# Performance work log

Hardware: AMD Instinct MI355X
Metric: run time of the kernel (lower is better)

## Reference

```python
import jax, jax.numpy as jnp
import numpy as np

N, E, H, RBF, NZ = 15000, 300000, 128, 20, 119
CUTOFF, BOX = 6.0, 7.0


def setup_inputs() -> dict:
    key = jax.random.key(0)
    ks = jax.random.split(key, 24)
    s = 0.05

    def rn(k, shape):
        return jax.random.normal(k, shape, dtype=jnp.float32) * s

    z = jax.random.randint(ks[0], (N,), 0, 83)
    pos = jax.random.uniform(ks[1], (N, 3), dtype=jnp.float32) * BOX
    src = jax.random.randint(ks[2], (E,), 0, N)
    dst = (src + jax.random.randint(ks[3], (E,), 1, N)) % N  # guarantees src != dst
    edge_index = jnp.stack([src, dst], axis=0)  # (2, E)
    cell_offsets = (jax.random.randint(ks[4], (E, 3), 0, 3) - 1).astype(jnp.float32)
    cell = jnp.eye(3, dtype=jnp.float32) * BOX
    return dict(
        z=z, pos=pos, edge_index=edge_index, cell_offsets=cell_offsets, cell=cell,
        embed=rn(ks[5], (NZ, H)),
        msg_w1=rn(ks[6], (3, H, H)), msg_b1=rn(ks[7], (3, H)),
        msg_w2=rn(ks[8], (3, H, 3 * H)), msg_b2=rn(ks[9], (3, 3 * H)),
        filt_w=rn(ks[10], (3, RBF, 3 * H)), filt_b=rn(ks[11], (3, 3 * H)),
        upd_uw=rn(ks[12], (3, H, H)), upd_ub=rn(ks[13], (3, H)),
        upd_vw=rn(ks[14], (3, H, H)), upd_vb=rn(ks[15], (3, H)),
        upd_mw1=rn(ks[16], (3, 2 * H, H)), upd_mb1=rn(ks[17], (3, H)),
        upd_mw2=rn(ks[18], (3, H, 3 * H)), upd_mb2=rn(ks[19], (3, 3 * H)),
        head_w1=rn(ks[20], (H, H)), head_b1=rn(ks[21], (H,)),
        head_w2=rn(ks[22], (H, H)), head_b2=rn(ks[23], (H,)),
    )


def reference(z, pos, edge_index, cell_offsets, cell, embed,
              msg_w1, msg_b1, msg_w2, msg_b2, filt_w, filt_b,
              upd_uw, upd_ub, upd_vw, upd_vb,
              upd_mw1, upd_mb1, upd_mw2, upd_mb2,
              head_w1, head_b1, head_w2, head_b2):
    n_nodes = z.shape[0]
    hdim = embed.shape[1]
    row, col = edge_index[0], edge_index[1]  # receiver, sender (DeepDFT convention)

    # get_pbc_distances
    offsets = cell_offsets @ cell                                  # (E,3)
    edge_diff = pos[row] - pos[col] + offsets                      # (E,3)
    edge_dist = jnp.linalg.norm(edge_diff, axis=-1)                # (E,)
    unit = edge_diff / edge_dist[:, None]                          # (E,3)

    # sinc radial basis + cosine cutoff (shared by all message layers)
    n = jnp.arange(1, RBF + 1, dtype=pos.dtype)
    rbf = jnp.sin(edge_dist[:, None] * n * jnp.pi / CUTOFF) / edge_dist[:, None]  # (E,RBF)
    fcut = jnp.where(edge_dist < CUTOFF,
                     0.5 * (jnp.cos(jnp.pi * edge_dist / CUTOFF) + 1.0), 0.0)      # (E,)

    ns = embed[z]                                                  # (N,H)
    nv = jnp.zeros((n_nodes, 3, hdim), dtype=pos.dtype)            # (N,3,H)

    for i in range(3):
        # ---- PainnMessage ----
        filt = (rbf @ filt_w[i] + filt_b[i]) * fcut[:, None]       # (E,3H)
        sout = jax.nn.silu(ns @ msg_w1[i] + msg_b1[i]) @ msg_w2[i] + msg_b2[i]  # (N,3H)
        fo = filt * sout[col]                                      # (E,3H)
        gate_v, gate_e, msg_s = jnp.split(fo, 3, axis=1)           # each (E,H)
        msg_v = nv[col] * gate_v[:, None, :] + gate_e[:, None, :] * unit[:, :, None]  # (E,3,H)
        ns = ns + jax.ops.segment_sum(msg_s, row, num_segments=n_nodes)
        nv = nv + jax.ops.segment_sum(msg_v, row, num_segments=n_nodes)
        # ---- PainnUpdate ----
        Uv = nv @ upd_uw[i] + upd_ub[i]                            # (N,3,H)
        Vv = nv @ upd_vw[i] + upd_vb[i]                            # (N,3,H)
        mlp_in = jnp.concatenate([jnp.linalg.norm(Vv, axis=1), ns], axis=1)  # (N,2H)
        m = jax.nn.silu(mlp_in @ upd_mw1[i] + upd_mb1[i]) @ upd_mw2[i] + upd_mb2[i]  # (N,3H)
        a_vv, a_sv, a_ss = jnp.split(m, 3, axis=1)
        inner = jnp.sum(Uv * Vv, axis=1)                           # (N,H)
        nv = nv + a_vv[:, None, :] * Uv
        ns = ns + a_sv * inner + a_ss

    v = jax.nn.silu(ns @ head_w1 + head_b1) @ head_w2 + head_b2    # (N,H)
    return v, edge_dist
```

## Files before the change

kernel.cpp:

```cpp
#include <hip/hip_runtime.h>
#include <math.h>

#define HD 128
#define H3 384
#define RBF_N 20
#define CUTOFF_R 6.0f
#define PI_F 3.14159265358979323846f
#define CAPE 40000

#define PITCH 136

typedef __attribute__((ext_vector_type(8))) short short8v;
typedef __attribute__((ext_vector_type(4))) short short4v;
typedef __attribute__((ext_vector_type(4))) float f32x4;
typedef unsigned short bf_t;

__device__ __forceinline__ float silu_f(float x) { return x / (1.0f + __expf(-x)); }

__device__ __forceinline__ ushort f2bf(float f) {
    union { float f; uint u; } v; v.f = f;
    return (ushort)((v.u + 0x7FFF + ((v.u >> 16) & 1)) >> 16);
}
__device__ __forceinline__ float bf2f(ushort x) {
    union { uint u; float f; } v; v.u = ((uint)x) << 16;
    return v.f;
}
__device__ __forceinline__ short4v f2bf4(float4 x) {
    short4v r;
    r[0] = (short)f2bf(x.x); r[1] = (short)f2bf(x.y);
    r[2] = (short)f2bf(x.z); r[3] = (short)f2bf(x.w);
    return r;
}
__device__ __forceinline__ float4 b2f4(short4v x) {
    return make_float4(bf2f((ushort)x[0]), bf2f((ushort)x[1]),
                       bf2f((ushort)x[2]), bf2f((ushort)x[3]));
}

#define LOADWG(r, CNT, NTH, W, rowlen, koff)                                   \
    _Pragma("unroll")                                                          \
    for (int it_ = 0; it_ < CNT; ++it_) {                                      \
        int u_ = tid + it_ * NTH;                                              \
        (r)[it_] = *(const short8v*)((W) + (size_t)(u_ >> 4) * (rowlen) +      \
                                     (koff) + ((u_ & 15) << 3));               \
    }
#define COMMITWG(r, CNT, NTH)                                                  \
    _Pragma("unroll")                                                          \
    for (int it_ = 0; it_ < CNT; ++it_) {                                      \
        int u_ = tid + it_ * NTH;                                              \
        *(short8v*)&Wt[(u_ >> 4) * PITCH + ((u_ & 15) << 3)] = (r)[it_];       \
    }
#define MFMA4R(Abuf, acc)                                                      \
    _Pragma("unroll")                                                          \
    for (int step_ = 0; step_ < 4; ++step_) {                                  \
        int kb_ = step_ * 32 + lk;                                             \
        short8v a_ = *(const short8v*)&(Abuf)[(wr + lr) * PITCH + kb_];        \
        (acc) = __builtin_amdgcn_mfma_f32_16x16x32_bf16(                       \
            a_, *(const short8v*)&Wt[(wn + lr) * PITCH + kb_], (acc), 0, 0, 0);\
    }
#define MFMA8R(Abuf, acc)                                                      \
    _Pragma("unroll")                                                          \
    for (int step_ = 0; step_ < 4; ++step_) {                                  \
        int kb_ = step_ * 32 + lk;                                             \
        short8v a_ = *(const short8v*)&(Abuf)[(wr + lr) * PITCH + kb_];        \
        (acc)[0] = __builtin_amdgcn_mfma_f32_16x16x32_bf16(                    \
            a_, *(const short8v*)&Wt[(wn + lr) * PITCH + kb_], (acc)[0], 0, 0, 0); \
        (acc)[1] = __builtin_amdgcn_mfma_f32_16x16x32_bf16(                    \
            a_, *(const short8v*)&Wt[(wn + 16 + lr) * PITCH + kb_], (acc)[1], 0, 0, 0); \
    }

__global__ void geom_kernel(const float* __restrict__ pos, const int* __restrict__ ei,
                            const float* __restrict__ cofs, const float* __restrict__ cell,
                            float* __restrict__ dist_out, int* __restrict__ deg, int E) {
    int e = blockIdx.x * blockDim.x + threadIdx.x;
    if (e >= E) return;
    int r = ei[e], c = ei[E + e];
    float c0 = cofs[3*e], c1 = cofs[3*e+1], c2 = cofs[3*e+2];
    float d0 = pos[3*r]   - pos[3*c]   + c0*cell[0] + c1*cell[3] + c2*cell[6];
    float d1 = pos[3*r+1] - pos[3*c+1] + c0*cell[1] + c1*cell[4] + c2*cell[7];
    float d2 = pos[3*r+2] - pos[3*c+2] + c0*cell[2] + c1*cell[5] + c2*cell[8];
    float dist = sqrtf(d0*d0 + d1*d1 + d2*d2);
    dist_out[e] = dist;
    if (dist < CUTOFF_R) atomicAdd(&deg[r], 1);
}

__global__ void scan_kernel(const int* __restrict__ deg, int* __restrict__ off,
                            int* __restrict__ cursor, int n) {
    __shared__ int wsum[16];
    __shared__ int carry_s;
    const int tid = threadIdx.x;
    const int lane = tid & 63, wv = tid >> 6;
    if (tid == 0) carry_s = 0;
    __syncthreads();
    for (int base = 0; base < n; base += 1024) {
        int v = (base + tid < n) ? deg[base + tid] : 0;
        int x = v;
        #pragma unroll
        for (int s = 1; s < 64; s <<= 1) {
            int y = __shfl_up(x, s);
            if (lane >= s) x += y;
        }
        if (lane == 63) wsum[wv] = x;
        __syncthreads();
        if (tid == 0) {
            int a = carry_s;
            #pragma unroll
            for (int i = 0; i < 16; ++i) { int t = wsum[i]; wsum[i] = a; a += t; }
            carry_s = a;
        }
        __syncthreads();
        int exc = wsum[wv] + x - v;
        if (base + tid < n) { off[base + tid] = exc; cursor[base + tid] = exc; }
        __syncthreads();
    }
    if (tid == 0) off[n] = carry_s;
}

__global__ void scatter_kernel(const float* __restrict__ pos, const int* __restrict__ ei,
                               const float* __restrict__ cofs, const float* __restrict__ cell,
                               const float* __restrict__ dist_in, int* __restrict__ cursor,
                               int* __restrict__ col_s, float* __restrict__ fcut_s,
                               float* __restrict__ unit_s, float* __restrict__ rbf_s, int E) {
    int e = blockIdx.x * blockDim.x + threadIdx.x;
    if (e >= E) return;
    float dist = dist_in[e];
    if (!(dist < CUTOFF_R)) return;
    int r = ei[e], c = ei[E + e];
    float c0 = cofs[3*e], c1 = cofs[3*e+1], c2 = cofs[3*e+2];
    float d0 = pos[3*r]   - pos[3*c]   + c0*cell[0] + c1*cell[3] + c2*cell[6];
    float d1 = pos[3*r+1] - pos[3*c+1] + c0*cell[1] + c1*cell[4] + c2*cell[7];
    float d2 = pos[3*r+2] - pos[3*c+2] + c0*cell[2] + c1*cell[5] + c2*cell[8];
    int p = atomicAdd(&cursor[r], 1);
    if (p >= CAPE) return;
    col_s[p] = c;
    fcut_s[p] = 0.5f * (cosf(PI_F * dist / CUTOFF_R) + 1.0f);
    float inv = 1.0f / dist;
    unit_s[3*p]   = d0 * inv;
    unit_s[3*p+1] = d1 * inv;
    unit_s[3*p+2] = d2 * inv;
    #pragma unroll
    for (int j = 0; j < RBF_N; ++j)
        rbf_s[(size_t)p*RBF_N + j] = sinf(dist * (float)(j+1) * (PI_F / CUTOFF_R)) * inv;
}

__device__ __forceinline__ void wcvt(const float* __restrict__ src, bf_t* __restrict__ dst,
                                     int idx, int K, int N) {
    int per = K * N;
    int l = idx / per, r = idx % per;
    int k = r / N, n = r % N;
    dst[(size_t)l*per + (size_t)n*K + k] = f2bf(src[(size_t)l*per + (size_t)k*N + n]);
}

__global__ void wprep_kernel(const float* s0, const float* s1, const float* s2, const float* s3,
                             const float* s4, const float* s5, const float* s6, const float* s7,
                             bf_t* __restrict__ dst) {
    int i = blockIdx.x * blockDim.x + threadIdx.x;
    if (i < 49152)        wcvt(s0, dst + 0,      i - 0,      128, 128);
    else if (i < 196608)  wcvt(s1, dst + 49152,  i - 49152,  128, 384);
    else if (i < 245760)  wcvt(s2, dst + 196608, i - 196608, 128, 128);
    else if (i < 294912)  wcvt(s3, dst + 245760, i - 245760, 128, 128);
    else if (i < 393216)  wcvt(s4, dst + 294912, i - 294912, 256, 128);
    else if (i < 540672)  wcvt(s5, dst + 393216, i - 393216, 128, 384);
    else if (i < 557056)  wcvt(s6, dst + 540672, i - 540672, 128, 128);
    else if (i < 573440)  wcvt(s7, dst + 557056, i - 557056, 128, 128);
}

__global__ __launch_bounds__(512) void msg_mlp0(const int* __restrict__ z,
                                                const float* __restrict__ emb,
                                                bf_t* __restrict__ nsb,
                                                const bf_t* __restrict__ W1b,
                                                const float* __restrict__ b1,
                                                const bf_t* __restrict__ W2b,
                                                const float* __restrict__ b2,
                                                bf_t* __restrict__ Cb, int M) {
    __shared__ ushort As[32 * PITCH];
    __shared__ ushort Wt[128 * PITCH];
    __shared__ ushort Hid[32 * PITCH];
    const int tid = threadIdx.x;
    const int m0 = blockIdx.x * 32;
    const int wid = tid >> 6, lane = tid & 63;
    const int wr = (wid >> 2) * 16;
    const int wn = (wid & 3) * 32;
    const int lr = lane & 15, lk = (lane >> 4) << 3;
    const int er = (lane >> 4) << 2;

    short8v rwA[4], rwB[4];
    LOADWG(rwA, 4, 512, W1b, 128, 0);
    {
        int row = tid >> 4, k8 = (tid & 15) << 3;
        int m = m0 + row;
        short8v pk = (short8v)(0);
        if (m < M) {
            const float* ep = emb + (size_t)z[m] * HD + k8;
            const float4 x = *(const float4*)ep, y = *(const float4*)(ep + 4);
            pk[0]=(short)f2bf(x.x); pk[1]=(short)f2bf(x.y);
            pk[2]=(short)f2bf(x.z); pk[3]=(short)f2bf(x.w);
            pk[4]=(short)f2bf(y.x); pk[5]=(short)f2bf(y.y);
            pk[6]=(short)f2bf(y.z); pk[7]=(short)f2bf(y.w);
            *(short8v*)(nsb + (size_t)m * HD + k8) = pk;
        }
        *(short8v*)&As[row * PITCH + k8] = pk;
    }
    __syncthreads();
    COMMITWG(rwA, 4, 512); LOADWG(rwB, 4, 512, W2b, 128, 0);
    __syncthreads();
    f32x4 acc1[2];
    acc1[0] = (f32x4)(0.f); acc1[1] = (f32x4)(0.f);
    MFMA8R(As, acc1);
    __syncthreads();
    COMMITWG(rwB, 4, 512); LOADWG(rwA, 4, 512, W2b + 16384, 128, 0);
    #pragma unroll
    for (int j = 0; j < 2; ++j) {
        int col = wn + 16 * j + lr;
        float bb = b1[col];
        #pragma unroll
        for (int r = 0; r < 4; ++r)
            Hid[(wr + er + r) * PITCH + col] = f2bf(silu_f(acc1[j][r] + bb));
    }
    __syncthreads();
    {
        f32x4 a0[2]; a0[0] = (f32x4)(0.f); a0[1] = (f32x4)(0.f);
        MFMA8R(Hid, a0);
        __syncthreads();
        COMMITWG(rwA, 4, 512); LOADWG(rwB, 4, 512, W2b + 32768, 128, 0);
        #pragma unroll
        for (int j = 0; j < 2; ++j) {
            int col = wn + 16 * j + lr;
            float bb = b2[col];
            #pragma unroll
            for (int r = 0; r < 4; ++r) {
                int m = m0 + wr + er + r;
                if (m < M) Cb[(size_t)m * H3 + col] = f2bf(a0[j][r] + bb);
            }
        }
        __syncthreads();
    }
    {
        f32x4 a1[2]; a1[0] = (f32x4)(0.f); a1[1] = (f32x4)(0.f);
        MFMA8R(Hid, a1);
        __syncthreads();
        COMMITWG(rwB, 4, 512);
        #pragma unroll
        for (int j = 0; j < 2; ++j) {
            int col = wn + 16 * j + lr;
            float bb = b2[128 + col];
            #pragma unroll
            for (int r = 0; r < 4; ++r) {
                int m = m0 + wr + er + r;
                if (m < M) Cb[(size_t)m * H3 + 128 + col] = f2bf(a1[j][r] + bb);
            }
        }
        __syncthreads();
    }
    {
        f32x4 a2[2]; a2[0] = (f32x4)(0.f); a2[1] = (f32x4)(0.f);
        MFMA8R(Hid, a2);
        #pragma unroll
        for (int j = 0; j < 2; ++j) {
            int col = wn + 16 * j + lr;
            float bb = b2[256 + col];
            #pragma unroll
            for (int r = 0; r < 4; ++r) {
                int m = m0 + wr + er + r;
                if (m < M) Cb[(size_t)m * H3 + 256 + col] = f2bf(a2[j][r] + bb);
            }
        }
    }
}

template <int MODE>
__global__ __launch_bounds__(1024) void upd_fused(const bf_t* __restrict__ nv2p,
                                                 const bf_t* __restrict__ Ub,
                                                 const bf_t* __restrict__ Vb,
                                                 const float* __restrict__ bu,
                                                 const float* __restrict__ bv,
                                                 bf_t* __restrict__ nvp,
                                                 bf_t* __restrict__ nsb,
                                                 const bf_t* __restrict__ W1b,
                                                 const float* __restrict__ b1,
                                                 const bf_t* __restrict__ W2b,
                                                 const float* __restrict__ b2,
                                                 const bf_t* __restrict__ xw1,
                                                 const float* __restrict__ xb1,
                                                 const bf_t* __restrict__ xw2,
                                                 const float* __restrict__ xb2,
                                                 bf_t* __restrict__ soutb,
                                                 float* __restrict__ Cf,
                                                 int N) {
    __shared__ ushort As3[3][32 * PITCH];
    __shared__ ushort Wt[128 * PITCH];
    __shared__ ushort nrmL[32 * PITCH];
    __shared__ ushort Hid[32 * PITCH];
    __shared__ ushort AsG[32 * PITCH];
    const int tid = threadIdx.x;
    const int m0 = blockIdx.x * 32;
    const int wid = tid >> 6, lane = tid & 63;
    const int wr = (wid >> 3) * 16;
    const int wn = (wid & 7) * 16;
    const int lr = lane & 15, lk = (lane >> 4) << 3;
    const int er = (lane >> 4) << 2;
    const size_t NHD = (size_t)N * HD;

    short8v rwA[2], rwB[2];
    LOADWG(rwA, 2, 1024, Ub, 128, 0);

    #pragma unroll
    for (int it = 0; it < 2; ++it) {
        int u = tid + it * 1024;
        if (u < 1536) {
            int d = u >> 9, v = u & 511;
            int row = v >> 4, k8 = (v & 15) << 3;
            int m = m0 + row;
            short8v pk = (short8v)(0);
            if (m < N) pk = *(const short8v*)(nv2p + (size_t)d * NHD + (size_t)m * HD + k8);
            *(short8v*)&As3[d][row * PITCH + k8] = pk;
        }
    }
    if (tid < 512) {
        int row = tid >> 4, k8 = (tid & 15) << 3;
        int m = m0 + row;
        short8v pk = (short8v)(0);
        if (m < N) pk = *(const short8v*)(nsb + (size_t)m * HD + k8);
        *(short8v*)&AsG[row * PITCH + k8] = pk;
    }
    __syncthreads();
    COMMITWG(rwA, 2, 1024); LOADWG(rwB, 2, 1024, Vb, 128, 0);
    __syncthreads();

    f32x4 aU[3], aV[3];
    #pragma unroll
    for (int d = 0; d < 3; ++d) { aU[d] = (f32x4)(0.f); aV[d] = (f32x4)(0.f); }
    #pragma unroll
    for (int d = 0; d < 3; ++d) { MFMA4R(As3[d], aU[d]); }
    __syncthreads();
    COMMITWG(rwB, 2, 1024); LOADWG(rwA, 2, 1024, W1b, 256, 0);
    __syncthreads();

    #pragma unroll
    for (int d = 0; d < 3; ++d) { MFMA4R(As3[d], aV[d]); }
    float inn_r[4];
    {
        int col = wn + lr;
        float bbu = bu[col], bbv = bv[col];
        #pragma unroll
        for (int r = 0; r < 4; ++r) {
            float inn = 0.f, nrm = 0.f;
            #pragma unroll
            for (int d = 0; d < 3; ++d) {
                float u = aU[d][r] + bbu;
                float v = aV[d][r] + bbv;
                aU[d][r] = u;
                inn += u * v;
                nrm += v * v;
            }
            inn_r[r] = inn;
            nrmL[(wr + er + r) * PITCH + col] = f2bf(sqrtf(nrm));
        }
    }
    __syncthreads();
    COMMITWG(rwA, 2, 1024); LOADWG(rwB, 2, 1024, W1b, 256, 128);
    __syncthreads();

    f32x4 acc1 = (f32x4)(0.f);
    MFMA4R(nrmL, acc1);
    __syncthreads();
    COMMITWG(rwB, 2, 1024);
    if (MODE == 1) { LOADWG(rwA, 2, 1024, W2b, 128, 0); }
    else           { LOADWG(rwA, 2, 1024, W2b + 16384, 128, 0); }
    __syncthreads();

    MFMA4R(AsG, acc1);
    {
        int col = wn + lr;
        float bb = b1[col];
        #pragma unroll
        for (int r = 0; r < 4; ++r)
            Hid[(wr + er + r) * PITCH + col] = f2bf(silu_f(acc1[r] + bb));
    }
    __syncthreads();
    COMMITWG(rwA, 2, 1024);
    if (MODE == 1) { LOADWG(rwB, 2, 1024, W2b + 16384, 128, 0); }
    else           { LOADWG(rwB, 2, 1024, W2b + 32768, 128, 0); }
    __syncthreads();

    float sv[4];
    if (MODE == 1) {
        f32x4 g0 = (f32x4)(0.f);
        MFMA4R(Hid, g0);
        {
            int col = wn + lr;
            float bb = b2[col];
            #pragma unroll
            for (int r = 0; r < 4; ++r) {
                int m = m0 + wr + er + r;
                if (m < N) {
                    float g = g0[r] + bb;
                    #pragma unroll
                    for (int d = 0; d < 3; ++d) {
                        float pp = bf2f(As3[d][(wr + er + r) * PITCH + col]);
                        nvp[(size_t)d * NHD + (size_t)m * HD + col] =
                            f2bf(pp + g * aU[d][r]);
                    }
                }
            }
        }
        __syncthreads();
        COMMITWG(rwB, 2, 1024); LOADWG(rwA, 2, 1024, W2b + 32768, 128, 0);
        __syncthreads();
        f32x4 g1 = (f32x4)(0.f);
        MFMA4R(Hid, g1);
        {
            int col = wn + lr;
            float bb = b2[128 + col];
            #pragma unroll
            for (int r = 0; r < 4; ++r)
                sv[r] = (g1[r] + bb) * inn_r[r];
        }
        __syncthreads();
        COMMITWG(rwA, 2, 1024); LOADWG(rwB, 2, 1024, xw1, 128, 0);
        __syncthreads();
        f32x4 g2 = (f32x4)(0.f);
        MFMA4R(Hid, g2);
        {
            int col = wn + lr;
            float bb = b2[256 + col];
            #pragma unroll
            for (int r = 0; r < 4; ++r) {
                int m = m0 + wr + er + r;
                if (m < N) {
                    int idx = (wr + er + r) * PITCH + col;
                    float s = bf2f(AsG[idx]) + sv[r] + (g2[r] + bb);
                    ushort sb = f2bf(s);
                    AsG[idx] = sb;
                    nsb[(size_t)m * HD + col] = sb;
                }
            }
        }
        __syncthreads();
        COMMITWG(rwB, 2, 1024); LOADWG(rwA, 2, 1024, xw2, 128, 0);
        __syncthreads();
        f32x4 ah = (f32x4)(0.f);
        MFMA4R(AsG, ah);
        {
            int col = wn + lr;
            float bb = xb1[col];
            #pragma unroll
            for (int r = 0; r < 4; ++r)
                Hid[(wr + er + r) * PITCH + col] = f2bf(silu_f(ah[r] + bb));
        }
        __syncthreads();
        COMMITWG(rwA, 2, 1024); LOADWG(rwB, 2, 1024, xw2 + 16384, 128, 0);
        __syncthreads();
        {
            f32x4 o0 = (f32x4)(0.f);
            MFMA4R(Hid, o0);
            int col = wn + lr;
            float bb = xb2[col];
            #pragma unroll
            for (int r = 0; r < 4; ++r) {
                int m = m0 + wr + er + r;
                if (m < N) soutb[(size_t)m * H3 + col] = f2bf(o0[r] + bb);
            }
        }
        __syncthreads();
        COMMITWG(rwB, 2, 1024); LOADWG(rwA, 2, 1024, xw2 + 32768, 128, 0);
        __syncthreads();
        {
            f32x4 o1 = (f32x4)(0.f);
            MFMA4R(Hid, o1);
            int col = wn + lr;
            float bb = xb2[128 + col];
            #pragma unroll
            for (int r = 0; r < 4; ++r) {
                int m = m0 + wr + er + r;
                if (m < N) soutb[(size_t)m * H3 + 128 + col] = f2bf(o1[r] + bb);
            }
        }
        __syncthreads();
        COMMITWG(rwA, 2, 1024);
        __syncthreads();
        {
            f32x4 o2 = (f32x4)(0.f);
            MFMA4R(Hid, o2);
            int col = wn + lr;
            float bb = xb2[256 + col];
            #pragma unroll
            for (int r = 0; r < 4; ++r) {
                int m = m0 + wr + er + r;
                if (m < N) soutb[(size_t)m * H3 + 256 + col] = f2bf(o2[r] + bb);
            }
        }
    } else {
        f32x4 g1 = (f32x4)(0.f);
        MFMA4R(Hid, g1);
        {
            int col = wn + lr;
            float bb = b2[128 + col];
            #pragma unroll
            for (int r = 0; r < 4; ++r)
                sv[r] = (g1[r] + bb) * inn_r[r];
        }
        __syncthreads();
        COMMITWG(rwB, 2, 1024); LOADWG(rwA, 2, 1024, xw1, 128, 0);
        __syncthreads();
        f32x4 g2 = (f32x4)(0.f);
        MFMA4R(Hid, g2);
        {
            int col = wn + lr;
            float bb = b2[256 + col];
            #pragma unroll
            for (int r = 0; r < 4; ++r) {
                int idx = (wr + er + r) * PITCH + col;
                float s = bf2f(AsG[idx]) + sv[r] + (g2[r] + bb);
                AsG[idx] = f2bf(s);
            }
        }
        __syncthreads();
        COMMITWG(rwA, 2, 1024); LOADWG(rwB, 2, 1024, xw2, 128, 0);
        __syncthreads();
        f32x4 ah = (f32x4)(0.f);
        MFMA4R(AsG, ah);
        {
            int col = wn + lr;
            float bb = xb1[col];
            #pragma unroll
            for (int r = 0; r < 4; ++r)
                Hid[(wr + er + r) * PITCH + col] = f2bf(silu_f(ah[r] + bb));
        }
        __syncthreads();
        COMMITWG(rwB, 2, 1024);
        __syncthreads();
        f32x4 ao = (f32x4)(0.f);
        MFMA4R(Hid, ao);
        {
            int col = wn + lr;
            float bb = xb2[col];
            #pragma unroll
            for (int r = 0; r < 4; ++r) {
                int m = m0 + wr + er + r;
                if (m < N) Cf[(size_t)m * HD + col] = ao[r] + bb;
            }
        }
    }
}

template <int FIRST>
__global__ __launch_bounds__(128) void message_kernel(
        bf_t* __restrict__ ns_b,
        const bf_t* __restrict__ nv_b, bf_t* __restrict__ nv2_b,
        const bf_t* __restrict__ sout,
        const int* __restrict__ col_s, const float* __restrict__ unit_s,
        const float* __restrict__ rbf_s, const float* __restrict__ fcut_s,
        const float* __restrict__ Wf_g, const float* __restrict__ bf_g,
        const int* __restrict__ off, int n_nodes) {
    const int t = threadIdx.x;
    const int nA = blockIdx.x * 2;
    if (nA >= n_nodes) return;
    const int nB = nA + 1;
    const bool hasB = (nB < n_nodes);
    const size_t NHD = (size_t)n_nodes * HD;

    float w0[RBF_N], w1[RBF_N], w2[RBF_N];
    #pragma unroll
    for (int r = 0; r < RBF_N; ++r) {
        w0[r] = Wf_g[r * H3 + t];
        w1[r] = Wf_g[r * H3 + HD + t];
        w2[r] = Wf_g[r * H3 + 2*HD + t];
    }
    const float bb0 = bf_g[t], bb1 = bf_g[HD + t], bb2 = bf_g[2*HD + t];

    int e0   = off[nA];
    int endA = off[nA + 1];
    int end  = hasB ? off[nB + 1] : endA;
    if (endA > CAPE) endA = CAPE;
    if (end  > CAPE) end  = CAPE;

    float aS = 0.f, a0 = 0.f, a1 = 0.f, a2 = 0.f;
    float bS = 0.f, b0 = 0.f, b1 = 0.f, b2 = 0.f;

    int e = e0;
    for (; e + 1 < end; e += 2) {
        int cX = col_s[e], cY = col_s[e + 1];
        float fcX = fcut_s[e], fcY = fcut_s[e + 1];
        float uX0 = unit_s[3*e],   uX1 = unit_s[3*e+1], uX2 = unit_s[3*e+2];
        float uY0 = unit_s[3*e+3], uY1 = unit_s[3*e+4], uY2 = unit_s[3*e+5];
        float fX0 = bb0, fX1 = bb1, fX2 = bb2;
        float fY0 = bb0, fY1 = bb1, fY2 = bb2;
        const float* rbX = rbf_s + (size_t)e * RBF_N;
        const float* rbY = rbX + RBF_N;
        #pragma unroll
        for (int r = 0; r < RBF_N; ++r) {
            float rx = rbX[r], ry = rbY[r];
            fX0 += rx * w0[r]; fY0 += ry * w0[r];
            fX1 += rx * w1[r]; fY1 += ry * w1[r];
            fX2 += rx * w2[r]; fY2 += ry * w2[r];
        }
        const bf_t* spX = sout + (size_t)cX * H3;
        const bf_t* spY = sout + (size_t)cY * H3;
        float gvX = fX0 * fcX * bf2f(spX[t]);
        float geX = fX1 * fcX * bf2f(spX[HD+t]);
        float msX = fX2 * fcX * bf2f(spX[2*HD+t]);
        float gvY = fY0 * fcY * bf2f(spY[t]);
        float geY = fY1 * fcY * bf2f(spY[HD+t]);
        float msY = fY2 * fcY * bf2f(spY[2*HD+t]);
        float vX0, vX1, vX2, vY0, vY1, vY2;
        if (FIRST) {
            vX0 = geX * uX0; vX1 = geX * uX1; vX2 = geX * uX2;
            vY0 = geY * uY0; vY1 = geY * uY1; vY2 = geY * uY2;
        } else {
            const bf_t* nvX = nv_b + (size_t)cX * HD + t;
            const bf_t* nvY = nv_b + (size_t)cY * HD + t;
            vX0 = bf2f(nvX[0])     * gvX + geX * uX0;
            vX1 = bf2f(nvX[NHD])   * gvX + geX * uX1;
            vX2 = bf2f(nvX[2*NHD]) * gvX + geX * uX2;
            vY0 = bf2f(nvY[0])     * gvY + geY * uY0;
            vY1 = bf2f(nvY[NHD])   * gvY + geY * uY1;
            vY2 = bf2f(nvY[2*NHD]) * gvY + geY * uY2;
        }
        if (e < endA) { a0 += vX0; a1 += vX1; a2 += vX2; aS += msX; }
        else          { b0 += vX0; b1 += vX1; b2 += vX2; bS += msX; }
        if (e + 1 < endA) { a0 += vY0; a1 += vY1; a2 += vY2; aS += msY; }
        else              { b0 += vY0; b1 += vY1; b2 += vY2; bS += msY; }
    }
    if (e < end) {
        int c = col_s[e];
        float fc = fcut_s[e];
        float u0 = unit_s[3*e], u1 = unit_s[3*e+1], u2 = unit_s[3*e+2];
        float f0 = bb0, f1 = bb1, f2 = bb2;
        const float* rb = rbf_s + (size_t)e * RBF_N;
        #pragma unroll
        for (int r = 0; r < RBF_N; ++r) {
            float rv = rb[r];
            f0 += rv * w0[r];
            f1 += rv * w1[r];
            f2 += rv * w2[r];
        }
        const bf_t* sp = sout + (size_t)c * H3;
        float gv = f0 * fc * bf2f(sp[t]);
        float ge = f1 * fc * bf2f(sp[HD+t]);
        float ms = f2 * fc * bf2f(sp[2*HD+t]);
        float v0, v1, v2;
        if (FIRST) {
            v0 = ge * u0; v1 = ge * u1; v2 = ge * u2;
        } else {
            const bf_t* nvc = nv_b + (size_t)c * HD + t;
            v0 = bf2f(nvc[0])     * gv + ge * u0;
            v1 = bf2f(nvc[NHD])   * gv + ge * u1;
            v2 = bf2f(nvc[2*NHD]) * gv + ge * u2;
        }
        if (e < endA) { a0 += v0; a1 += v1; a2 += v2; aS += ms; }
        else          { b0 += v0; b1 += v1; b2 += v2; bS += ms; }
    }

    {
        size_t b = (size_t)nA * HD + t;
        if (FIRST) {
            nv2_b[b]         = f2bf(a0);
            nv2_b[b + NHD]   = f2bf(a1);
            nv2_b[b + 2*NHD] = f2bf(a2);
        } else {
            nv2_b[b]         = f2bf(bf2f(nv_b[b])         + a0);
            nv2_b[b + NHD]   = f2bf(bf2f(nv_b[b + NHD])   + a1);
            nv2_b[b + 2*NHD] = f2bf(bf2f(nv_b[b + 2*NHD]) + a2);
        }
        if (endA > e0) {
            size_t so = (size_t)nA * HD + t;
            ns_b[so] = f2bf(bf2f(ns_b[so]) + aS);
        }
    }
    if (hasB) {
        size_t b = (size_t)nB * HD + t;
        if (FIRST) {
            nv2_b[b]         = f2bf(b0);
            nv2_b[b + NHD]   = f2bf(b1);
            nv2_b[b + 2*NHD] = f2bf(b2);
        } else {
            nv2_b[b]         = f2bf(bf2f(nv_b[b])         + b0);
            nv2_b[b + NHD]   = f2bf(bf2f(nv_b[b + NHD])   + b1);
            nv2_b[b + 2*NHD] = f2bf(bf2f(nv_b[b + 2*NHD]) + b2);
        }
        if (end > endA) {
            size_t so = (size_t)nB * HD + t;
            ns_b[so] = f2bf(bf2f(ns_b[so]) + bS);
        }
    }
}

extern "C" void kernel_launch(void* const* d_in, const int* in_sizes, int n_in,
                              void* d_out, int out_size, void* d_ws, size_t ws_size,
                              hipStream_t stream) {
    const int*   z       = (const int*)  d_in[0];
    const float* pos     = (const float*)d_in[1];
    const int*   ei      = (const int*)  d_in[2];
    const float* cofs    = (const float*)d_in[3];
    const float* cell    = (const float*)d_in[4];
    const float* emb     = (const float*)d_in[5];
    const float* msg_w1  = (const float*)d_in[6];
    const float* msg_b1  = (const float*)d_in[7];
    const float* msg_w2  = (const float*)d_in[8];
    const float* msg_b2  = (const float*)d_in[9];
    const float* filt_w  = (const float*)d_in[10];
    const float* filt_b  = (const float*)d_in[11];
    const float* upd_uw  = (const float*)d_in[12];
    const float* upd_ub  = (const float*)d_in[13];
    const float* upd_vw  = (const float*)d_in[14];
    const float* upd_vb  = (const float*)d_in[15];
    const float* upd_mw1 = (const float*)d_in[16];
    const float* upd_mb1 = (const float*)d_in[17];
    const float* upd_mw2 = (const float*)d_in[18];
    const float* upd_mb2 = (const float*)d_in[19];
    const float* head_w1 = (const float*)d_in[20];
    const float* head_b1 = (const float*)d_in[21];
    const float* head_w2 = (const float*)d_in[22];
    const float* head_b2 = (const float*)d_in[23];

    const int N = in_sizes[0];
    const int E = in_sizes[2] / 2;

    float* out_v    = (float*)d_out;
    float* out_dist = out_v + (size_t)N * HD;

    char* p = (char*)d_ws;
    auto alloc = [&](size_t bytes) -> void* {
        void* r = (void*)p;
        p += (bytes + 255) & ~(size_t)255;
        return r;
    };
    bf_t*  ns_b   = (bf_t*) alloc((size_t)N * HD * 2);
    bf_t*  nv_b   = (bf_t*) alloc((size_t)N * H3 * 2);
    bf_t*  nv2_b  = (bf_t*) alloc((size_t)N * H3 * 2);
    bf_t*  sout   = (bf_t*) alloc((size_t)N * H3 * 2);
    bf_t*  wb     = (bf_t*) alloc((size_t)573440 * 2);
    float* rbf_s  = (float*)alloc((size_t)CAPE * RBF_N * 4);
    float* fcut_s = (float*)alloc((size_t)CAPE * 4);
    float* unit_s = (float*)alloc((size_t)CAPE * 3 * 4);
    int*   col_s  = (int*)  alloc((size_t)CAPE * 4);
    int*   deg    = (int*)  alloc((size_t)N * 4);
    int*   off    = (int*)  alloc((size_t)(N + 1) * 4);
    int*   cursor = (int*)  alloc((size_t)N * 4);

    hipMemsetAsync(deg, 0, (size_t)N * 4, stream);

    int eb = (E + 255) / 256;
    geom_kernel<<<eb, 256, 0, stream>>>(pos, ei, cofs, cell, out_dist, deg, E);
    scan_kernel<<<1, 1024, 0, stream>>>(deg, off, cursor, N);
    scatter_kernel<<<eb, 256, 0, stream>>>(pos, ei, cofs, cell, out_dist, cursor,
                                           col_s, fcut_s, unit_s, rbf_s, E);
    wprep_kernel<<<(573440 + 255) / 256, 256, 0, stream>>>(
        msg_w1, msg_w2, upd_uw, upd_vw, upd_mw1, upd_mw2, head_w1, head_w2, wb);

    const bf_t* w_msg1 = wb + 0;
    const bf_t* w_msg2 = wb + 49152;
    const bf_t* w_uw   = wb + 196608;
    const bf_t* w_vw   = wb + 245760;
    const bf_t* w_mw1  = wb + 294912;
    const bf_t* w_mw2  = wb + 393216;
    const bf_t* w_hw1  = wb + 540672;
    const bf_t* w_hw2  = wb + 557056;

    int mt32 = (N + 31) / 32;
    int mpairs = (N + 1) / 2;

    msg_mlp0<<<mt32, 512, 0, stream>>>(
        z, emb, ns_b, w_msg1, msg_b1, w_msg2, msg_b2, sout, N);

    for (int i = 0; i < 3; ++i) {
        if (i == 0)
            message_kernel<1><<<mpairs, 128, 0, stream>>>(
                ns_b, nv_b, nv2_b, sout, col_s, unit_s, rbf_s, fcut_s,
                filt_w + (size_t)i*RBF_N*H3, filt_b + (size_t)i*H3, off, N);
        else
            message_kernel<0><<<mpairs, 128, 0, stream>>>(
                ns_b, nv_b, nv2_b, sout, col_s, unit_s, rbf_s, fcut_s,
                filt_w + (size_t)i*RBF_N*H3, filt_b + (size_t)i*H3, off, N);
        if (i < 2) {
            upd_fused<1><<<mt32, 1024, 0, stream>>>(
                nv2_b, w_uw + (size_t)i*16384, w_vw + (size_t)i*16384,
                upd_ub + (size_t)i*HD, upd_vb + (size_t)i*HD,
                nv_b, ns_b,
                w_mw1 + (size_t)i*32768, upd_mb1 + (size_t)i*HD,
                w_mw2 + (size_t)i*49152, upd_mb2 + (size_t)i*H3,
                w_msg1 + (size_t)(i+1)*16384, msg_b1 + (size_t)(i+1)*HD,
                w_msg2 + (size_t)(i+1)*49152, msg_b2 + (size_t)(i+1)*H3,
                sout, nullptr, N);
        } else {
            upd_fused<3><<<mt32, 1024, 0, stream>>>(
                nv2_b, w_uw + (size_t)i*16384, w_vw + (size_t)i*16384,
                upd_ub + (size_t)i*HD, upd_vb + (size_t)i*HD,
                nv_b, ns_b,
                w_mw1 + (size_t)i*32768, upd_mb1 + (size_t)i*HD,
                w_mw2 + (size_t)i*49152, upd_mb2 + (size_t)i*H3,
                w_hw1, head_b1, w_hw2, head_b2,
                nullptr, out_v, N);
        }
    }
}
```

Before: 225.5 us.

## Cache edge vectors, drop separate norm LDS buffer, store filter weights as bf16

```diff
diff --git a/kernel.cpp b/kernel.cpp
--- a/kernel.cpp
+++ b/kernel.cpp
@@ -70,7 +70,8 @@
 
 __global__ void geom_kernel(const float* __restrict__ pos, const int* __restrict__ ei,
                             const float* __restrict__ cofs, const float* __restrict__ cell,
-                            float* __restrict__ dist_out, int* __restrict__ deg, int E) {
+                            float* __restrict__ dist_out, float* __restrict__ dvec,
+                            int* __restrict__ deg, int E) {
     int e = blockIdx.x * blockDim.x + threadIdx.x;
     if (e >= E) return;
     int r = ei[e], c = ei[E + e];
@@ -80,7 +81,12 @@
     float d2 = pos[3*r+2] - pos[3*c+2] + c0*cell[2] + c1*cell[5] + c2*cell[8];
     float dist = sqrtf(d0*d0 + d1*d1 + d2*d2);
     dist_out[e] = dist;
-    if (dist < CUTOFF_R) atomicAdd(&deg[r], 1);
+    if (dist < CUTOFF_R) {
+        dvec[e]       = d0;
+        dvec[E + e]   = d1;
+        dvec[2*E + e] = d2;
+        atomicAdd(&deg[r], 1);
+    }
 }
 
 __global__ void scan_kernel(const int* __restrict__ deg, int* __restrict__ off,
@@ -115,9 +121,10 @@
     if (tid == 0) off[n] = carry_s;
 }
 
-__global__ void scatter_kernel(const float* __restrict__ pos, const int* __restrict__ ei,
-                               const float* __restrict__ cofs, const float* __restrict__ cell,
-                               const float* __restrict__ dist_in, int* __restrict__ cursor,
+__global__ void scatter_kernel(const int* __restrict__ ei,
+                               const float* __restrict__ dist_in,
+                               const float* __restrict__ dvec,
+                               int* __restrict__ cursor,
                                int* __restrict__ col_s, float* __restrict__ fcut_s,
                                float* __restrict__ unit_s, float* __restrict__ rbf_s, int E) {
     int e = blockIdx.x * blockDim.x + threadIdx.x;
@@ -125,10 +132,7 @@
     float dist = dist_in[e];
     if (!(dist < CUTOFF_R)) return;
     int r = ei[e], c = ei[E + e];
-    float c0 = cofs[3*e], c1 = cofs[3*e+1], c2 = cofs[3*e+2];
-    float d0 = pos[3*r]   - pos[3*c]   + c0*cell[0] + c1*cell[3] + c2*cell[6];
-    float d1 = pos[3*r+1] - pos[3*c+1] + c0*cell[1] + c1*cell[4] + c2*cell[7];
-    float d2 = pos[3*r+2] - pos[3*c+2] + c0*cell[2] + c1*cell[5] + c2*cell[8];
+    float d0 = dvec[e], d1 = dvec[E + e], d2 = dvec[2*E + e];
     int p = atomicAdd(&cursor[r], 1);
     if (p >= CAPE) return;
     col_s[p] = c;
@@ -152,6 +156,7 @@
 
 __global__ void wprep_kernel(const float* s0, const float* s1, const float* s2, const float* s3,
                              const float* s4, const float* s5, const float* s6, const float* s7,
+                             const float* s8,
                              bf_t* __restrict__ dst) {
     int i = blockIdx.x * blockDim.x + threadIdx.x;
     if (i < 49152)        wcvt(s0, dst + 0,      i - 0,      128, 128);
@@ -162,6 +167,7 @@
     else if (i < 540672)  wcvt(s5, dst + 393216, i - 393216, 128, 384);
     else if (i < 557056)  wcvt(s6, dst + 540672, i - 540672, 128, 128);
     else if (i < 573440)  wcvt(s7, dst + 557056, i - 557056, 128, 128);
+    else if (i < 596480)  dst[i] = f2bf(s8[i - 573440]);
 }
 
 __global__ __launch_bounds__(512) void msg_mlp0(const int* __restrict__ z,
@@ -288,7 +294,6 @@
                                                  int N) {
     __shared__ ushort As3[3][32 * PITCH];
     __shared__ ushort Wt[128 * PITCH];
-    __shared__ ushort nrmL[32 * PITCH];
     __shared__ ushort Hid[32 * PITCH];
     __shared__ ushort AsG[32 * PITCH];
     const int tid = threadIdx.x;
@@ -353,7 +358,7 @@
                 nrm += v * v;
             }
             inn_r[r] = inn;
-            nrmL[(wr + er + r) * PITCH + col] = f2bf(sqrtf(nrm));
+            Hid[(wr + er + r) * PITCH + col] = f2bf(sqrtf(nrm));
         }
     }
     __syncthreads();
@@ -361,7 +366,7 @@
     __syncthreads();
 
     f32x4 acc1 = (f32x4)(0.f);
-    MFMA4R(nrmL, acc1);
+    MFMA4R(Hid, acc1);
     __syncthreads();
     COMMITWG(rwB, 2, 1024);
     if (MODE == 1) { LOADWG(rwA, 2, 1024, W2b, 128, 0); }
@@ -440,6 +445,7 @@
         __syncthreads();
         f32x4 ah = (f32x4)(0.f);
         MFMA4R(AsG, ah);
+        __syncthreads();
         {
             int col = wn + lr;
             float bb = xb1[col];
@@ -519,6 +525,7 @@
         __syncthreads();
         f32x4 ah = (f32x4)(0.f);
         MFMA4R(AsG, ah);
+        __syncthreads();
         {
             int col = wn + lr;
             float bb = xb1[col];
@@ -550,7 +557,7 @@
         const bf_t* __restrict__ sout,
         const int* __restrict__ col_s, const float* __restrict__ unit_s,
         const float* __restrict__ rbf_s, const float* __restrict__ fcut_s,
-        const float* __restrict__ Wf_g, const float* __restrict__ bf_g,
+        const bf_t* __restrict__ Wf_b, const float* __restrict__ bf_g,
         const int* __restrict__ off, int n_nodes) {
     const int t = threadIdx.x;
     const int nA = blockIdx.x * 2;
@@ -562,9 +569,9 @@
     float w0[RBF_N], w1[RBF_N], w2[RBF_N];
     #pragma unroll
     for (int r = 0; r < RBF_N; ++r) {
-        w0[r] = Wf_g[r * H3 + t];
-        w1[r] = Wf_g[r * H3 + HD + t];
-        w2[r] = Wf_g[r * H3 + 2*HD + t];
+        w0[r] = bf2f(Wf_b[r * H3 + t]);
+        w1[r] = bf2f(Wf_b[r * H3 + HD + t]);
+        w2[r] = bf2f(Wf_b[r * H3 + 2*HD + t]);
     }
     const float bb0 = bf_g[t], bb1 = bf_g[HD + t], bb2 = bf_g[2*HD + t];
 
@@ -729,7 +736,8 @@
     bf_t*  nv_b   = (bf_t*) alloc((size_t)N * H3 * 2);
     bf_t*  nv2_b  = (bf_t*) alloc((size_t)N * H3 * 2);
     bf_t*  sout   = (bf_t*) alloc((size_t)N * H3 * 2);
-    bf_t*  wb     = (bf_t*) alloc((size_t)573440 * 2);
+    bf_t*  wb     = (bf_t*) alloc((size_t)596480 * 2);
+    float* dvec   = (float*)alloc((size_t)E * 3 * 4);
     float* rbf_s  = (float*)alloc((size_t)CAPE * RBF_N * 4);
     float* fcut_s = (float*)alloc((size_t)CAPE * 4);
     float* unit_s = (float*)alloc((size_t)CAPE * 3 * 4);
@@ -741,12 +749,12 @@
     hipMemsetAsync(deg, 0, (size_t)N * 4, stream);
 
     int eb = (E + 255) / 256;
-    geom_kernel<<<eb, 256, 0, stream>>>(pos, ei, cofs, cell, out_dist, deg, E);
+    geom_kernel<<<eb, 256, 0, stream>>>(pos, ei, cofs, cell, out_dist, dvec, deg, E);
     scan_kernel<<<1, 1024, 0, stream>>>(deg, off, cursor, N);
-    scatter_kernel<<<eb, 256, 0, stream>>>(pos, ei, cofs, cell, out_dist, cursor,
+    scatter_kernel<<<eb, 256, 0, stream>>>(ei, out_dist, dvec, cursor,
                                            col_s, fcut_s, unit_s, rbf_s, E);
-    wprep_kernel<<<(573440 + 255) / 256, 256, 0, stream>>>(
-        msg_w1, msg_w2, upd_uw, upd_vw, upd_mw1, upd_mw2, head_w1, head_w2, wb);
+    wprep_kernel<<<(596480 + 255) / 256, 256, 0, stream>>>(
+        msg_w1, msg_w2, upd_uw, upd_vw, upd_mw1, upd_mw2, head_w1, head_w2, filt_w, wb);
 
     const bf_t* w_msg1 = wb + 0;
     const bf_t* w_msg2 = wb + 49152;
@@ -756,6 +764,7 @@
     const bf_t* w_mw2  = wb + 393216;
     const bf_t* w_hw1  = wb + 540672;
     const bf_t* w_hw2  = wb + 557056;
+    const bf_t* w_fw   = wb + 573440;
 
     int mt32 = (N + 31) / 32;
     int mpairs = (N + 1) / 2;
@@ -767,11 +776,11 @@
         if (i == 0)
             message_kernel<1><<<mpairs, 128, 0, stream>>>(
                 ns_b, nv_b, nv2_b, sout, col_s, unit_s, rbf_s, fcut_s,
-                filt_w + (size_t)i*RBF_N*H3, filt_b + (size_t)i*H3, off, N);
+                w_fw + (size_t)i*RBF_N*H3, filt_b + (size_t)i*H3, off, N);
         else
             message_kernel<0><<<mpairs, 128, 0, stream>>>(
                 ns_b, nv_b, nv2_b, sout, col_s, unit_s, rbf_s, fcut_s,
-                filt_w + (size_t)i*RBF_N*H3, filt_b + (size_t)i*H3, off, N);
+                w_fw + (size_t)i*RBF_N*H3, filt_b + (size_t)i*H3, off, N);
         if (i < 2) {
             upd_fused<1><<<mt32, 1024, 0, stream>>>(
                 nv2_b, w_uw + (size_t)i*16384, w_vw + (size_t)i*16384,
```

New measurement: 224.6 us. About the same (-0.4%).
